# Kernel optimization log

Measured on AMD Instinct MI355X. Metric: run time of the kernel, lower is better.

The kernel has to match this reference:

```python
import jax, jax.numpy as jnp
import numpy as np

B, K, N, E, D = 32, 32, 2048, 16384, 768
L_GNN, L_TR, H = 2, 4, 12
FF, VOCAB, N_ROLES, MAX_POS, N_HOPS = 3072, 25, 2, 64, 16


def setup_inputs() -> dict:
    key = jax.random.key(0)
    ks = jax.random.split(key, 32)
    s = 0.02
    inp = {
        "raw_features": jax.random.normal(ks[0], (B, K, D), jnp.float32),
        "x0": jax.random.randint(ks[1], (K, N), 0, VOCAB),
        "edge0": jax.random.randint(ks[2], (K, 2, E), 0, N),
        "batch0": jnp.sort(jax.random.randint(ks[3], (K, N), 0, B), axis=-1),
        "x1": jax.random.randint(ks[4], (K, N), 0, VOCAB),
        "edge1": jax.random.randint(ks[5], (K, 2, E), 0, N),
        "batch1": jnp.sort(jax.random.randint(ks[6], (K, N), 0, B), axis=-1),
        "role_ids": jax.random.randint(ks[7], (B, K), 0, N_ROLES),
        "position_ids": jax.random.randint(ks[8], (B, K), 0, MAX_POS),
        "hop_ids": jax.random.randint(ks[9], (B, K), 0, N_HOPS),
        # GNNForProtein params (shared across slots and both proteins)
        "amino_embed": jax.random.normal(ks[10], (VOCAB, D)) * s,
        "gnn_W": jax.random.normal(ks[11], (L_GNN, D, D)) * s,
        "gnn_b": jnp.zeros((L_GNN, D)),
        # GraphBert embeddings
        "role_emb": jax.random.normal(ks[12], (N_ROLES, D)) * s,
        "pos_emb": jax.random.normal(ks[13], (MAX_POS, D)) * s,
        "hop_emb": jax.random.normal(ks[14], (N_HOPS, D)) * s,
        "emb_ln_scale": jnp.ones((D,)),
        "emb_ln_bias": jnp.zeros((D,)),
        # GraphBert transformer layers (stacked over L_TR)
        "Wq": jax.random.normal(ks[15], (L_TR, D, D)) * s,
        "bq": jnp.zeros((L_TR, D)),
        "Wk": jax.random.normal(ks[16], (L_TR, D, D)) * s,
        "bk": jnp.zeros((L_TR, D)),
        "Wv": jax.random.normal(ks[17], (L_TR, D, D)) * s,
        "bv": jnp.zeros((L_TR, D)),
        "Wo": jax.random.normal(ks[18], (L_TR, D, D)) * s,
        "bo": jnp.zeros((L_TR, D)),
        "ln1_s": jnp.ones((L_TR, D)),
        "ln1_b": jnp.zeros((L_TR, D)),
        "W1": jax.random.normal(ks[19], (L_TR, D, FF)) * s,
        "b1": jnp.zeros((L_TR, FF)),
        "W2": jax.random.normal(ks[20], (L_TR, FF, D)) * s,
        "b2": jnp.zeros((L_TR, D)),
        "ln2_s": jnp.ones((L_TR, D)),
        "ln2_b": jnp.zeros((L_TR, D)),
    }
    return inp


def _ln(x, s, b):
    m = jnp.mean(x, -1, keepdims=True)
    v = jnp.mean(jnp.square(x - m), -1, keepdims=True)
    return (x - m) * jax.lax.rsqrt(v + 1e-12) * s + b


def _gnn(node_ids, edges, batch_idx, amino_embed, W, b):
    # One protein slot: GCN message passing + mean readout per graph in batch.
    h = amino_embed[node_ids]                      # [N, D]
    src, dst = edges[0], edges[1]
    for l in range(W.shape[0]):
        agg = jax.ops.segment_sum(h[src], dst, num_segments=N)
        h = jax.nn.relu((h + agg) @ W[l] + b[l])
    sums = jax.ops.segment_sum(h, batch_idx, num_segments=B)
    cnt = jax.ops.segment_sum(jnp.ones((h.shape[0], 1), h.dtype), batch_idx, num_segments=B)
    return sums / jnp.maximum(cnt, 1.0)           # [B, D]


def reference(raw_features, x0, edge0, batch0, x1, edge1, batch1, role_ids, position_ids, hop_ids,
              amino_embed, gnn_W, gnn_b, role_emb, pos_emb, hop_emb, emb_ln_scale, emb_ln_bias,
              Wq, bq, Wk, bk, Wv, bv, Wo, bo, ln1_s, ln1_b, W1, b1, W2, b2, ln2_s, ln2_b):
    # vmap over the K protein slots replaces the original Python loop (same math).
    gnn_v = jax.vmap(_gnn, in_axes=(0, 0, 0, None, None, None))
    p0 = gnn_v(x0, edge0, batch0, amino_embed, gnn_W, gnn_b)   # [K, B, D]
    p1 = gnn_v(x1, edge1, batch1, amino_embed, gnn_W, gnn_b)   # [K, B, D]
    feats = raw_features + jnp.transpose(p0 + p1, (1, 0, 2))   # [B, K, D]
    # GraphBert embeddings + encoder
    h = feats + role_emb[role_ids] + pos_emb[position_ids] + hop_emb[hop_ids]
    h = _ln(h, emb_ln_scale, emb_ln_bias)
    dh = D // H
    scale = float(1.0 / np.sqrt(dh))
    for l in range(Wq.shape[0]):
        q = (h @ Wq[l] + bq[l]).reshape(B, K, H, dh)
        kk = (h @ Wk[l] + bk[l]).reshape(B, K, H, dh)
        v = (h @ Wv[l] + bv[l]).reshape(B, K, H, dh)
        att = jax.nn.softmax(jnp.einsum('bqhd,bkhd->bhqk', q, kk) * scale, axis=-1)
        ctx = jnp.einsum('bhqk,bkhd->bqhd', att, v).reshape(B, K, D)
        h = _ln(h + ctx @ Wo[l] + bo[l], ln1_s[l], ln1_b[l])
        f = jax.nn.gelu(h @ W1[l] + b1[l]) @ W2[l] + b2[l]
        h = _ln(h + f, ln2_s[l], ln2_b[l])
    return h
```

## Files before the change

kernel.cpp:

```cpp
#include <hip/hip_runtime.h>
#include <hip/hip_bf16.h>
#include <math.h>

using bf16 = __hip_bfloat16;
typedef __attribute__((ext_vector_type(8))) short short8;
typedef __attribute__((ext_vector_type(4))) float floatx4;
typedef __attribute__((ext_vector_type(4))) short short4v;

#define NB   32
#define NK   32
#define NNODE 2048
#define NEDGE 16384
#define ND   768
#define NHH  12
#define DHH  64
#define NFF  3072
#define NG   64
#define LTR  4
#define VOCAB 25

static __device__ __forceinline__ float b2f(bf16 x) { return __bfloat162float(x); }
static __device__ __forceinline__ bf16 f2b(float x) { return __float2bfloat16(x); }
static __device__ __forceinline__ float bs2f(short s) {
    unsigned u = ((unsigned)(unsigned short)s) << 16;
    float f; __builtin_memcpy(&f, &u, 4); return f;
}
static __device__ __forceinline__ short f2bs(float x) {
    bf16 h = f2b(x); short s; __builtin_memcpy(&s, &h, 2); return s;
}

static __device__ __forceinline__ void load_lds16(const bf16* g, bf16* l) {
    __builtin_amdgcn_global_load_lds((const __attribute__((address_space(1))) void*)g,
                                     (__attribute__((address_space(3))) void*)l, 16, 0, 0);
}

static __device__ __forceinline__ float ldf(const void* p, size_t i, bool f32) {
    return f32 ? ((const float*)p)[i] : b2f(((const bf16*)p)[i]);
}

__global__ void detect_dtype_kernel(const void* __restrict__ eln_s, int* __restrict__ flag) {
    if (threadIdx.x == 0 && blockIdx.x == 0) {
        unsigned w = ((const unsigned*)eln_s)[0];
        flag[0] = (w == 0x3F800000u) ? 1 : 0;
    }
}

__device__ __forceinline__ void conv_tile(const void* __restrict__ src, size_t srcOff,
                                          bf16* __restrict__ dst, int R, int Cn,
                                          int tr, int tc, bool f32, int t,
                                          bf16 (*tile)[65]) {
    int r0 = tr * 64, c0 = tc * 64;
    #pragma unroll
    for (int p = 0; p < 16; ++p) {
        int idx = t + p * 256;
        int r = idx >> 6, c = idx & 63;
        tile[r][c] = f2b(ldf(src, srcOff + (size_t)(r0 + r) * Cn + c0 + c, f32));
    }
    __syncthreads();
    #pragma unroll
    for (int p = 0; p < 16; ++p) {
        int idx = t + p * 256;
        int c = idx >> 6, r = idx & 63;
        dst[(size_t)(c0 + c) * R + r0 + r] = tile[r][c];
    }
}

__global__ __launch_bounds__(256) void convert_gnn_kernel(const void* __restrict__ gnnW,
                                                          bf16* __restrict__ gnnT,
                                                          const int* __restrict__ flag) {
    __shared__ bf16 tile[64][65];
    bool f32 = flag[0] != 0;
    int bid = blockIdx.x;
    int id = bid / 144, tl = bid % 144;
    conv_tile(gnnW, (size_t)id * 589824, gnnT + (size_t)id * 589824,
              768, 768, tl / 12, tl % 12, f32, threadIdx.x, tile);
}

__global__ __launch_bounds__(256) void convert_layer_kernel(
    const void* __restrict__ Wq, const void* __restrict__ Wk, const void* __restrict__ Wv,
    const void* __restrict__ Wo, const void* __restrict__ W1, const void* __restrict__ W2,
    int l, bf16* __restrict__ qkvT, bf16* __restrict__ oT,
    bf16* __restrict__ w1T, bf16* __restrict__ w2T, const int* __restrict__ flag) {
    __shared__ bf16 tile[64][65];
    bool f32 = flag[0] != 0;
    int bid = blockIdx.x, t = threadIdx.x;
    if (bid < 432) {
        int m = bid / 144, tl = bid % 144;
        const void* src = (m == 0) ? Wq : ((m == 1) ? Wk : Wv);
        conv_tile(src, (size_t)l * 589824, qkvT + (size_t)m * 589824,
                  768, 768, tl / 12, tl % 12, f32, t, tile);
    } else if (bid < 576) {
        int tl = bid - 432;
        conv_tile(Wo, (size_t)l * 589824, oT, 768, 768, tl / 12, tl % 12, f32, t, tile);
    } else if (bid < 1152) {
        int tl = bid - 576;
        conv_tile(W1, (size_t)l * 768 * 3072, w1T, 768, 3072, tl / 48, tl % 48, f32, t, tile);
    } else {
        int tl = bid - 1152;
        conv_tile(W2, (size_t)l * 3072 * 768, w2T, 3072, 768, tl / 12, tl % 12, f32, t, tile);
    }
}

__global__ __launch_bounds__(256) void pack_bias_kernel(
    const void* __restrict__ gnnb, const void* __restrict__ bq, const void* __restrict__ bk,
    const void* __restrict__ bv, const void* __restrict__ bo, const void* __restrict__ b1,
    const void* __restrict__ b2, float* __restrict__ out, const int* __restrict__ flag) {
    bool f32 = flag[0] != 0;
    int i = blockIdx.x * 256 + threadIdx.x;
    if (i >= 1536 + LTR * 6912) return;
    float v;
    if (i < 1536) v = ldf(gnnb, i, f32);
    else {
        int j = i - 1536, l = j / 6912, r = j % 6912;
        if      (r <  768) v = ldf(bq, l * 768 + r, f32);
        else if (r < 1536) v = ldf(bk, l * 768 + r - 768, f32);
        else if (r < 2304) v = ldf(bv, l * 768 + r - 1536, f32);
        else if (r < 3072) v = ldf(bo, l * 768 + r - 2304, f32);
        else if (r < 6144) v = ldf(b1, l * 3072 + r - 3072, f32);
        else               v = ldf(b2, l * 768 + r - 6144, f32);
    }
    out[i] = v;
}

__global__ __launch_bounds__(192) void e1_kernel(const void* __restrict__ emb,
                                                 const bf16* __restrict__ w0T,
                                                 bf16* __restrict__ E1,
                                                 const int* __restrict__ flag) {
    bool f32 = flag[0] != 0;
    int v = blockIdx.x, t = threadIdx.x;
    float acc[4] = {0.f, 0.f, 0.f, 0.f};
    for (int k = 0; k < ND; k += 4) {
        float e0 = ldf(emb, (size_t)v * ND + k,     f32);
        float e1 = ldf(emb, (size_t)v * ND + k + 1, f32);
        float e2 = ldf(emb, (size_t)v * ND + k + 2, f32);
        float e3 = ldf(emb, (size_t)v * ND + k + 3, f32);
        #pragma unroll
        for (int j = 0; j < 4; ++j) {
            const short4v w = *(const short4v*)&w0T[(size_t)(t * 4 + j) * ND + k];
            acc[j] += e0 * bs2f(w.x) + e1 * bs2f(w.y) + e2 * bs2f(w.z) + e3 * bs2f(w.w);
        }
    }
    short4v o; o.x = f2bs(acc[0]); o.y = f2bs(acc[1]); o.z = f2bs(acc[2]); o.w = f2bs(acc[3]);
    ((short4v*)(E1 + (size_t)v * ND))[t] = o;
}

__global__ __launch_bounds__(256) void count_deg_kernel(const int* __restrict__ edge0,
                                                        const int* __restrict__ edge1,
                                                        int* __restrict__ deg) {
    int gid = blockIdx.x;
    int g = gid >> 6, chunk = gid & 63;
    const int* ep = (g < NK) ? (edge0 + (size_t)g * 2 * NEDGE)
                             : (edge1 + (size_t)(g - NK) * 2 * NEDGE);
    int e = chunk * 256 + threadIdx.x;
    int dst = ep[NEDGE + e];
    atomicAdd(&deg[g * NNODE + dst], 1);
}

__global__ __launch_bounds__(256) void scan_deg_kernel(int* __restrict__ deg,
                                                       int* __restrict__ indptr) {
    int g = blockIdx.x, t = threadIdx.x;
    __shared__ int sums[256];
    int loc[8]; int s = 0;
    #pragma unroll
    for (int i = 0; i < 8; ++i) { loc[i] = deg[g * NNODE + t * 8 + i]; s += loc[i]; }
    sums[t] = s; __syncthreads();
    for (int off = 1; off < 256; off <<= 1) {
        int v = (t >= off) ? sums[t - off] : 0;
        __syncthreads();
        sums[t] += v;
        __syncthreads();
    }
    int run = sums[t] - s;
    #pragma unroll
    for (int i = 0; i < 8; ++i) {
        indptr[g * (NNODE + 1) + t * 8 + i] = run;
        deg[g * NNODE + t * 8 + i] = run;
        run += loc[i];
    }
    if (t == 255) indptr[g * (NNODE + 1) + NNODE] = run;
}

__global__ __launch_bounds__(256) void fill_csr_kernel(const int* __restrict__ edge0,
                                                       const int* __restrict__ edge1,
                                                       int* __restrict__ cursor,
                                                       int* __restrict__ csr_src) {
    int gid = blockIdx.x;
    int g = gid >> 6, chunk = gid & 63;
    const int* ep = (g < NK) ? (edge0 + (size_t)g * 2 * NEDGE)
                             : (edge1 + (size_t)(g - NK) * 2 * NEDGE);
    int e = chunk * 256 + threadIdx.x;
    int src = ep[e];
    int dst = ep[NEDGE + e];
    int p = atomicAdd(&cursor[g * NNODE + dst], 1);
    csr_src[(size_t)g * NEDGE + p] = src;
}

__global__ __launch_bounds__(64) void batch_count_kernel(const int* __restrict__ batch0,
                                                         const int* __restrict__ batch1,
                                                         int* __restrict__ cnt) {
    int g = blockIdx.x;
    int b = threadIdx.x;
    if (b >= NB) return;
    const int* bp = (g < NK) ? (batch0 + (size_t)g * NNODE)
                             : (batch1 + (size_t)(g - NK) * NNODE);
    int lo = 0, hi = NNODE;
    while (lo < hi) { int mid = (lo + hi) >> 1; if (bp[mid] < b) lo = mid + 1; else hi = mid; }
    int start = lo;
    hi = NNODE;
    while (lo < hi) { int mid = (lo + hi) >> 1; if (bp[mid] < b + 1) lo = mid + 1; else hi = mid; }
    cnt[g * NB + b] = lo - start;
}

static __device__ __forceinline__ void node_block_decode(int id, int& gl, int& n) {
    int r = id & 7, q = id >> 3;
    gl = r + 8 * (q >> 11);
    n = q & 2047;
}

__global__ __launch_bounds__(192) void gnn_layer1_kernel(const int* __restrict__ x0,
                                                         const int* __restrict__ x1,
                                                         const bf16* __restrict__ E1,
                                                         const float* __restrict__ b0,
                                                         const int* __restrict__ indptr,
                                                         const int* __restrict__ csr_src,
                                                         bf16* __restrict__ hC, int g0) {
    int gl, n; node_block_decode(blockIdx.x, gl, n);
    int g = g0 + gl;
    const int* xg = (g < NK) ? (x0 + (size_t)g * NNODE) : (x1 + (size_t)(g - NK) * NNODE);
    int beg = indptr[g * (NNODE + 1) + n];
    int end = indptr[g * (NNODE + 1) + n + 1];
    const int* cs = csr_src + (size_t)g * NEDGE;
    int t = threadIdx.x;
    const short4v* E = (const short4v*)E1;
    short4v v = E[(size_t)xg[n] * 192 + t];
    float a0 = bs2f(v.x), a1 = bs2f(v.y), a2 = bs2f(v.z), a3 = bs2f(v.w);
    for (int e = beg; e < end; ++e) {
        int s = cs[e];
        short4v w = E[(size_t)xg[s] * 192 + t];
        a0 += bs2f(w.x); a1 += bs2f(w.y); a2 += bs2f(w.z); a3 += bs2f(w.w);
    }
    float4 bb = ((const float4*)b0)[t];
    short4v o;
    o.x = f2bs(fmaxf(a0 + bb.x, 0.f));
    o.y = f2bs(fmaxf(a1 + bb.y, 0.f));
    o.z = f2bs(fmaxf(a2 + bb.z, 0.f));
    o.w = f2bs(fmaxf(a3 + bb.w, 0.f));
    ((short4v*)(hC + ((size_t)gl * NNODE + n) * ND))[t] = o;
}

__global__ __launch_bounds__(192) void gnn_aggregate_kernel(const bf16* __restrict__ hC,
                                                            const int* __restrict__ indptr,
                                                            const int* __restrict__ csr_src,
                                                            bf16* __restrict__ xC, int g0) {
    int gl, n; node_block_decode(blockIdx.x, gl, n);
    int g = g0 + gl;
    int beg = indptr[g * (NNODE + 1) + n];
    int end = indptr[g * (NNODE + 1) + n + 1];
    const short4v* hg = (const short4v*)(hC + (size_t)gl * NNODE * ND);
    const int* cs = csr_src + (size_t)g * NEDGE;
    int t = threadIdx.x;
    short4v v = hg[(size_t)n * 192 + t];
    float a0 = bs2f(v.x), a1 = bs2f(v.y), a2 = bs2f(v.z), a3 = bs2f(v.w);
    for (int e = beg; e < end; ++e) {
        int s = cs[e];
        short4v w = hg[(size_t)s * 192 + t];
        a0 += bs2f(w.x); a1 += bs2f(w.y); a2 += bs2f(w.z); a3 += bs2f(w.w);
    }
    short4v o; o.x = f2bs(a0); o.y = f2bs(a1); o.z = f2bs(a2); o.w = f2bs(a3);
    ((short4v*)(xC + ((size_t)gl * NNODE + n) * ND))[t] = o;
}

__global__ __launch_bounds__(256) void gemm_tn(const bf16* __restrict__ A,
                                               const bf16* __restrict__ BT,
                                               const float* __restrict__ bias,
                                               void* __restrict__ C,
                                               int M, int K, int N,
                                               int act, int outF32,
                                               const int* __restrict__ batAp,
                                               const int* __restrict__ batBp,
                                               float* __restrict__ pool, int g0) {
    __shared__ bf16 lA[2][128][32];
    __shared__ bf16 lB[2][128][32];
    int nTilesN = N >> 7, nTilesM = M >> 7;
    int brow, bcol;
    if ((nTilesM & 7) == 0) {
        int xcd = blockIdx.x & 7, j = blockIdx.x >> 3;
        brow = (j / nTilesN) * 8 + xcd;
        bcol = j % nTilesN;
    } else {
        bcol = blockIdx.x % nTilesN;
        brow = blockIdx.x / nTilesN;
    }
    int t = threadIdx.x;
    int wave = t >> 6, lane = t & 63;
    int wr = wave >> 1, wc = wave & 1;
    int l15 = lane & 15, quad = lane >> 4;
    const int row0 = brow << 7, col0 = bcol << 7;
    const int sr0 = t >> 2, sk0 = (t & 3) * 8;
    const bf16* Ab = A + (size_t)(row0 + sr0) * K + sk0;
    const bf16* Bb = BT + (size_t)(col0 + sr0) * K + sk0;
    const size_t rstride = (size_t)64 * K;

    load_lds16(Ab,           &lA[0][sr0][sk0]);
    load_lds16(Ab + rstride, &lA[0][sr0 + 64][sk0]);
    load_lds16(Bb,           &lB[0][sr0][sk0]);
    load_lds16(Bb + rstride, &lB[0][sr0 + 64][sk0]);

    floatx4 acc[4][4] = {};
    int cur = 0;
    for (int k0 = 0; k0 < K; k0 += 32) {
        __syncthreads();
        if (k0 + 32 < K) {
            load_lds16(Ab + k0 + 32,           &lA[cur ^ 1][sr0][sk0]);
            load_lds16(Ab + rstride + k0 + 32, &lA[cur ^ 1][sr0 + 64][sk0]);
            load_lds16(Bb + k0 + 32,           &lB[cur ^ 1][sr0][sk0]);
            load_lds16(Bb + rstride + k0 + 32, &lB[cur ^ 1][sr0 + 64][sk0]);
        }
        short8 afr[4], bfr[4];
        #pragma unroll
        for (int i = 0; i < 4; ++i)
            afr[i] = *reinterpret_cast<const short8*>(&lA[cur][wr * 64 + i * 16 + l15][quad * 8]);
        #pragma unroll
        for (int j = 0; j < 4; ++j)
            bfr[j] = *reinterpret_cast<const short8*>(&lB[cur][wc * 64 + j * 16 + l15][quad * 8]);
        #pragma unroll
        for (int i = 0; i < 4; ++i)
            #pragma unroll
            for (int j = 0; j < 4; ++j)
                acc[i][j] = __builtin_amdgcn_mfma_f32_16x16x32_bf16(afr[i], bfr[j], acc[i][j], 0, 0, 0);
        cur ^= 1;
    }

    if (pool) {
        int g = g0 + (row0 >> 11);
        const int* bp = (g < NK) ? (batAp + (size_t)g * NNODE)
                                 : (batBp + (size_t)(g - NK) * NNODE);
        int nbase = row0 & (NNODE - 1);
        float* pg = pool + (size_t)g * NB * ND;
        int cb = wc * 64 + l15;
        float bv[4];
        #pragma unroll
        for (int j = 0; j < 4; ++j) bv[j] = bias[col0 + cb + j * 16];
        __syncthreads();
        float* lp = (float*)lA;
        int bLo = bp[nbase], bHi = bp[nbase + 127];
        int nb = (bHi - bLo + 1) * 128;
        for (int idx = t; idx < nb; idx += 256) lp[idx] = 0.f;
        __syncthreads();
        float sums[4] = {0.f, 0.f, 0.f, 0.f};
        int curb = -1;
        #pragma unroll
        for (int i = 0; i < 4; ++i) {
            int rr = nbase + wr * 64 + i * 16 + quad * 4;
            #pragma unroll
            for (int r = 0; r < 4; ++r) {
                int b = bp[rr + r];
                if (b != curb) {
                    if (curb >= 0) {
                        #pragma unroll
                        for (int j = 0; j < 4; ++j)
                            atomicAdd(&lp[(curb - bLo) * 128 + cb + j * 16], sums[j]);
                    }
                    curb = b;
                    sums[0] = sums[1] = sums[2] = sums[3] = 0.f;
                }
                #pragma unroll
                for (int j = 0; j < 4; ++j) {
                    float v = acc[i][j][r] + bv[j];
                    if (act == 1) v = fmaxf(v, 0.f);
                    sums[j] += v;
                }
            }
        }
        #pragma unroll
        for (int j = 0; j < 4; ++j)
            atomicAdd(&lp[(curb - bLo) * 128 + cb + j * 16], sums[j]);
        __syncthreads();
        for (int idx = t; idx < nb; idx += 256) {
            float v = lp[idx];
            if (v != 0.f)
                atomicAdd(&pg[(size_t)(bLo + (idx >> 7)) * ND + col0 + (idx & 127)], v);
        }
        return;
    }

    #pragma unroll
    for (int i = 0; i < 4; ++i) {
        int rbase = row0 + wr * 64 + i * 16 + quad * 4;
        #pragma unroll
        for (int j = 0; j < 4; ++j) {
            int c = col0 + wc * 64 + j * 16 + l15;
            float bv = bias[c];
            #pragma unroll
            for (int r = 0; r < 4; ++r) {
                float v = acc[i][j][r] + bv;
                if (act == 1) v = fmaxf(v, 0.f);
                else if (act == 2) {
                    float x = v;
                    float u = 1.5957691216057308f * (x + 0.044715f * x * x * x);
                    v = x / (1.f + __expf(-u));
                }
                size_t idx = (size_t)(rbase + r) * N + c;
                if (outF32) ((float*)C)[idx] = v;
                else        ((bf16*)C)[idx] = f2b(v);
            }
        }
    }
}

__global__ __launch_bounds__(256) void gemm_tn_sk(const bf16* __restrict__ A,
                                                  const bf16* __restrict__ BT,
                                                  const float* __restrict__ bias,
                                                  float* __restrict__ C,
                                                  int M, int K, int N, int splitK) {
    __shared__ bf16 lA[2][64][32];
    __shared__ bf16 lB[2][128][32];
    int nTilesN = N >> 7, nTilesM = M >> 6;
    int tiles = nTilesM * nTilesN;
    int split = blockIdx.x / tiles;
    int jt = blockIdx.x % tiles;
    int brow = jt / nTilesN, bcol = jt % nTilesN;
    int t = threadIdx.x;
    int wave = t >> 6, lane = t & 63;
    int wr = wave >> 1, wc = wave & 1;
    int l15 = lane & 15, quad = lane >> 4;
    const int row0 = brow << 6, col0 = bcol << 7;
    const int kLen = K / splitK, kBeg = split * kLen;
    const int sr0 = t >> 2, sk0 = (t & 3) * 8;
    const bf16* Ab = A + (size_t)(row0 + sr0) * K + kBeg + sk0;
    const bf16* Bb = BT + (size_t)(col0 + sr0) * K + kBeg + sk0;
    const size_t rstride = (size_t)64 * K;

    load_lds16(Ab,           &lA[0][sr0][sk0]);
    load_lds16(Bb,           &lB[0][sr0][sk0]);
    load_lds16(Bb + rstride, &lB[0][sr0 + 64][sk0]);

    floatx4 acc[2][4] = {};
    int cur = 0;
    for (int k0 = 0; k0 < kLen; k0 += 32) {
        __syncthreads();
        if (k0 + 32 < kLen) {
            load_lds16(Ab + k0 + 32,           &lA[cur ^ 1][sr0][sk0]);
            load_lds16(Bb + k0 + 32,           &lB[cur ^ 1][sr0][sk0]);
            load_lds16(Bb + rstride + k0 + 32, &lB[cur ^ 1][sr0 + 64][sk0]);
        }
        short8 afr[2], bfr[4];
        #pragma unroll
        for (int i = 0; i < 2; ++i)
            afr[i] = *reinterpret_cast<const short8*>(&lA[cur][wr * 32 + i * 16 + l15][quad * 8]);
        #pragma unroll
        for (int j = 0; j < 4; ++j)
            bfr[j] = *reinterpret_cast<const short8*>(&lB[cur][wc * 64 + j * 16 + l15][quad * 8]);
        #pragma unroll
        for (int i = 0; i < 2; ++i)
            #pragma unroll
            for (int j = 0; j < 4; ++j)
                acc[i][j] = __builtin_amdgcn_mfma_f32_16x16x32_bf16(afr[i], bfr[j], acc[i][j], 0, 0, 0);
        cur ^= 1;
    }
    #pragma unroll
    for (int i = 0; i < 2; ++i) {
        int rbase = row0 + wr * 32 + i * 16 + quad * 4;
        #pragma unroll
        for (int j = 0; j < 4; ++j) {
            int c = col0 + wc * 64 + j * 16 + l15;
            float bv = (split == 0) ? bias[c] : 0.f;
            #pragma unroll
            for (int r = 0; r < 4; ++r)
                atomicAdd(&C[(size_t)(rbase + r) * N + c], acc[i][j][r] + bv);
        }
    }
}

__device__ __forceinline__ void block_ln_768(float (&x)[3], int t,
                                             const void* __restrict__ s,
                                             const void* __restrict__ b,
                                             size_t sOff, bool f32,
                                             float (&y)[3], float* red) {
    float loc = x[0] + x[1] + x[2];
    red[t] = loc; __syncthreads();
    for (int off = 128; off > 0; off >>= 1) {
        if (t < off) red[t] += red[t + off];
        __syncthreads();
    }
    float mean = red[0] * (1.f / 768.f);
    __syncthreads();
    float vs = 0.f;
    #pragma unroll
    for (int e = 0; e < 3; ++e) { float d = x[e] - mean; vs += d * d; }
    red[t] = vs; __syncthreads();
    for (int off = 128; off > 0; off >>= 1) {
        if (t < off) red[t] += red[t + off];
        __syncthreads();
    }
    float var = red[0] * (1.f / 768.f);
    __syncthreads();
    float inv = rsqrtf(var + 1e-12f);
    #pragma unroll
    for (int e = 0; e < 3; ++e) {
        int d = t + e * 256;
        y[e] = (x[e] - mean) * inv * ldf(s, sOff + d, f32) + ldf(b, sOff + d, f32);
    }
}

__global__ __launch_bounds__(256) void combine_embed_ln_kernel(
    const void* __restrict__ raw, const float* __restrict__ pooled,
    const int* __restrict__ cnt,
    const int* __restrict__ role_ids, const int* __restrict__ pos_ids, const int* __restrict__ hop_ids,
    const void* __restrict__ role_emb, const void* __restrict__ pos_emb, const void* __restrict__ hop_emb,
    const void* __restrict__ lns, const void* __restrict__ lnb,
    float* __restrict__ hT, bf16* __restrict__ hbf,
    const int* __restrict__ flag) {
    bool f32 = flag[0] != 0;
    __shared__ float red[256];
    int token = blockIdx.x;
    int b = token >> 5, k = token & 31;
    int t = threadIdx.x;
    int rid = role_ids[b * NK + k];
    int pid = pos_ids[b * NK + k];
    int hid = hop_ids[b * NK + k];
    float inv0 = 1.f / (float)max(cnt[k * NB + b], 1);
    float inv1 = 1.f / (float)max(cnt[(NK + k) * NB + b], 1);
    float x[3], y[3];
    #pragma unroll
    for (int e = 0; e < 3; ++e) {
        int d = t + e * 256;
        float p0 = pooled[((size_t)k * NB + b) * ND + d] * inv0;
        float p1 = pooled[((size_t)(NK + k) * NB + b) * ND + d] * inv1;
        x[e] = ldf(raw, (size_t)token * ND + d, f32) + p0 + p1
             + ldf(role_emb, (size_t)rid * ND + d, f32)
             + ldf(pos_emb, (size_t)pid * ND + d, f32)
             + ldf(hop_emb, (size_t)hid * ND + d, f32);
    }
    block_ln_768(x, t, lns, lnb, 0, f32, y, red);
    #pragma unroll
    for (int e = 0; e < 3; ++e) {
        int d = t + e * 256;
        hT[(size_t)token * ND + d] = y[e];
        hbf[(size_t)token * ND + d] = f2b(y[e]);
    }
}

__global__ __launch_bounds__(256) void add_ln_kernel(float* __restrict__ hT,
                                                     const float* __restrict__ addv,
                                                     const void* __restrict__ lns,
                                                     const void* __restrict__ lnb,
                                                     unsigned long long sOff,
                                                     void* __restrict__ outp, int extOut,
                                                     const int* __restrict__ flag) {
    bool f32 = flag[0] != 0;
    __shared__ float red[256];
    int token = blockIdx.x;
    int t = threadIdx.x;
    float x[3], y[3];
    #pragma unroll
    for (int e = 0; e < 3; ++e) {
        int d = t + e * 256;
        x[e] = hT[(size_t)token * ND + d] + addv[(size_t)token * ND + d];
    }
    block_ln_768(x, t, lns, lnb, sOff, f32, y, red);
    #pragma unroll
    for (int e = 0; e < 3; ++e) {
        int d = t + e * 256;
        size_t idx = (size_t)token * ND + d;
        hT[idx] = y[e];
        if (extOut && f32) ((float*)outp)[idx] = y[e];
        else               ((bf16*)outp)[idx] = f2b(y[e]);
    }
}

__global__ __launch_bounds__(256) void attn_kernel(const bf16* __restrict__ qkv,
                                                   bf16* __restrict__ ctx) {
    int blk = blockIdx.x;
    int b = blk / NHH, h = blk % NHH;
    __shared__ float lq[NK][DHH], lk[NK][DHH], lv[NK][DHH];
    __shared__ float ls[NK][NK];
    int t = threadIdx.x;
    for (int i = t; i < NK * DHH; i += 256) {
        int tok = i >> 6, d = i & 63;
        size_t base = ((size_t)(b * NK + tok)) * (3 * ND) + h * DHH + d;
        lq[tok][d] = b2f(qkv[base]);
        lk[tok][d] = b2f(qkv[base + ND]);
        lv[tok][d] = b2f(qkv[base + 2 * ND]);
    }
    __syncthreads();
    const float scale = 0.125f;
    for (int i = t; i < NK * NK; i += 256) {
        int qi = i >> 5, kj = i & 31;
        float s = 0.f;
        #pragma unroll
        for (int d = 0; d < DHH; ++d) s += lq[qi][d] * lk[kj][d];
        ls[qi][kj] = s * scale;
    }
    __syncthreads();
    if (t < NK) {
        float m = -1e30f;
        for (int j = 0; j < NK; ++j) m = fmaxf(m, ls[t][j]);
        float sum = 0.f;
        for (int j = 0; j < NK; ++j) { float e = expf(ls[t][j] - m); ls[t][j] = e; sum += e; }
        float inv = 1.f / sum;
        for (int j = 0; j < NK; ++j) ls[t][j] *= inv;
    }
    __syncthreads();
    for (int i = t; i < NK * DHH; i += 256) {
        int qi = i >> 6, d = i & 63;
        float s = 0.f;
        #pragma unroll
        for (int j = 0; j < NK; ++j) s += ls[qi][j] * lv[j][d];
        ctx[((size_t)(b * NK + qi)) * ND + h * DHH + d] = f2b(s);
    }
}

extern "C" void kernel_launch(void* const* d_in, const int* in_sizes, int n_in,
                              void* d_out, int out_size, void* d_ws, size_t ws_size,
                              hipStream_t stream) {
    const void* raw      = d_in[0];
    const int*  x0       = (const int*)d_in[1];
    const int*  edge0    = (const int*)d_in[2];
    const int*  batch0   = (const int*)d_in[3];
    const int*  x1       = (const int*)d_in[4];
    const int*  edge1    = (const int*)d_in[5];
    const int*  batch1   = (const int*)d_in[6];
    const int*  role_ids = (const int*)d_in[7];
    const int*  pos_ids  = (const int*)d_in[8];
    const int*  hop_ids  = (const int*)d_in[9];
    const void* amino    = d_in[10];
    const void* gnnW     = d_in[11];
    const void* gnnb     = d_in[12];
    const void* role_emb = d_in[13];
    const void* pos_emb  = d_in[14];
    const void* hop_emb  = d_in[15];
    const void* eln_s    = d_in[16];
    const void* eln_b    = d_in[17];
    const void* Wq       = d_in[18];
    const void* bq       = d_in[19];
    const void* Wk       = d_in[20];
    const void* bk       = d_in[21];
    const void* Wv       = d_in[22];
    const void* bv       = d_in[23];
    const void* Wo       = d_in[24];
    const void* bo       = d_in[25];
    const void* ln1_s    = d_in[26];
    const void* ln1_b    = d_in[27];
    const void* W1       = d_in[28];
    const void* b1       = d_in[29];
    const void* W2       = d_in[30];
    const void* b2       = d_in[31];
    const void* ln2_s    = d_in[32];
    const void* ln2_b    = d_in[33];

    char* ws = (char*)d_ws;
    size_t off = 0;
    auto alloc = [&](size_t bytes) -> void* {
        void* p = ws + off;
        off = (off + bytes + 255) & ~(size_t)255;
        return p;
    };
    int*   dflag   = (int*)alloc(256);
    float* pooled  = (float*)alloc((size_t)NG * NB * ND * 4);
    int*   cntb    = (int*)alloc((size_t)NG * NB * 4);
    int*   indptr  = (int*)alloc((size_t)NG * (NNODE + 1) * 4);
    int*   csr_src = (int*)alloc((size_t)NG * NEDGE * 4);
    int*   degcur  = (int*)alloc((size_t)NG * NNODE * 4);
    bf16*  gnnT    = (bf16*)alloc((size_t)2 * ND * ND * 2);
    bf16*  E1      = (bf16*)alloc((size_t)VOCAB * ND * 2);
    float* biasPk  = (float*)alloc((size_t)(1536 + LTR * 6912) * 4);

    const size_t QS = (size_t)3 * ND * ND, OS = (size_t)ND * ND;
    const size_t S1 = (size_t)ND * NFF,    S2 = (size_t)NFF * ND;
    const size_t wPerLayer = (QS + OS + S1 + S2) * 2;
    const size_t perG  = (size_t)NNODE * ND * 2;
    const size_t bigTR = 21 * 1024 * 1024;
    int gc = 8, nlw = 1;
    for (int cand = 32; cand >= 8; cand >>= 1) {
        size_t bigGNN = 2 * (size_t)cand * perG;
        size_t big = bigGNN > bigTR ? bigGNN : bigTR;
        if (off + 4 * wPerLayer + big + (1 << 20) <= ws_size) { gc = cand; nlw = 4; break; }
        if (off + wPerLayer + big + (1 << 20) <= ws_size)     { gc = cand; nlw = 1; break; }
    }
    bf16* qkvT = (bf16*)alloc(QS * 2 * nlw);
    bf16* oT   = (bf16*)alloc(OS * 2 * nlw);
    bf16* w1T  = (bf16*)alloc(S1 * 2 * nlw);
    bf16* w2T  = (bf16*)alloc(S2 * 2 * nlw);

    char* bigbase = (char*)alloc(2 * (size_t)gc * perG > bigTR ? 2 * (size_t)gc * perG : bigTR);
    bf16* hC = (bf16*)bigbase;
    bf16* xC = (bf16*)(bigbase + (size_t)gc * perG);
    size_t toff = 0;
    auto talloc = [&](size_t bytes) -> void* {
        void* p = bigbase + toff;
        toff = (toff + bytes + 255) & ~(size_t)255;
        return p;
    };
    float* hT    = (float*)talloc((size_t)NB * NK * ND * 4);
    bf16*  hbf   = (bf16*)talloc((size_t)NB * NK * ND * 2);
    bf16*  qkvb  = (bf16*)talloc((size_t)NB * NK * 3 * ND * 2);
    bf16*  ctxb  = (bf16*)talloc((size_t)NB * NK * ND * 2);
    float* resid = (float*)talloc((size_t)NB * NK * ND * 4);
    bf16*  ffbuf = (bf16*)talloc((size_t)NB * NK * NFF * 2);

    auto gemm = [&](const bf16* A, const bf16* BT, const float* bias, void* C,
                    int Mm, int Kk, int Nn, int act, int outF32) {
        int blocks = (Mm >> 7) * (Nn >> 7);
        gemm_tn<<<blocks, 256, 0, stream>>>(A, BT, bias, C, Mm, Kk, Nn, act, outF32,
                                            nullptr, nullptr, nullptr, 0);
    };
    auto gemm_sk = [&](const bf16* A, const bf16* BT, const float* bias, float* C,
                       int Mm, int Kk, int Nn, int splitK) {
        hipMemsetAsync(C, 0, (size_t)Mm * Nn * 4, stream);
        int blocks = (Mm >> 6) * (Nn >> 7) * splitK;
        gemm_tn_sk<<<blocks, 256, 0, stream>>>(A, BT, bias, C, Mm, Kk, Nn, splitK);
    };

    detect_dtype_kernel<<<1, 64, 0, stream>>>(eln_s, dflag);

    convert_gnn_kernel<<<288, 256, 0, stream>>>(gnnW, gnnT, dflag);
    pack_bias_kernel<<<(1536 + LTR * 6912 + 255) / 256, 256, 0, stream>>>(
        gnnb, bq, bk, bv, bo, b1, b2, biasPk, dflag);
    e1_kernel<<<VOCAB, 192, 0, stream>>>(amino, gnnT, E1, dflag);
    if (nlw == 4)
        for (int l = 0; l < LTR; ++l)
            convert_layer_kernel<<<1728, 256, 0, stream>>>(
                Wq, Wk, Wv, Wo, W1, W2, l,
                qkvT + (size_t)l * QS, oT + (size_t)l * OS,
                w1T + (size_t)l * S1, w2T + (size_t)l * S2, dflag);

    hipMemsetAsync(degcur, 0, (size_t)NG * NNODE * 4, stream);
    hipMemsetAsync(pooled, 0, (size_t)NG * NB * ND * 4, stream);
    count_deg_kernel<<<NG * 64, 256, 0, stream>>>(edge0, edge1, degcur);
    scan_deg_kernel<<<NG, 256, 0, stream>>>(degcur, indptr);
    fill_csr_kernel<<<NG * 64, 256, 0, stream>>>(edge0, edge1, degcur, csr_src);
    batch_count_kernel<<<NG, 64, 0, stream>>>(batch0, batch1, cntb);

    for (int g0 = 0; g0 < NG; g0 += gc) {
        gnn_layer1_kernel<<<gc * NNODE, 192, 0, stream>>>(x0, x1, E1, biasPk,
                                                          indptr, csr_src, hC, g0);
        gnn_aggregate_kernel<<<gc * NNODE, 192, 0, stream>>>(hC, indptr, csr_src, xC, g0);
        int blocks = ((gc * NNODE) >> 7) * (ND >> 7);
        gemm_tn<<<blocks, 256, 0, stream>>>(xC, gnnT + (size_t)ND * ND, biasPk + ND, nullptr,
                                            gc * NNODE, ND, ND, 1, 0,
                                            batch0, batch1, pooled, g0);
    }

    combine_embed_ln_kernel<<<NB * NK, 256, 0, stream>>>(
        raw, pooled, cntb, role_ids, pos_ids, hop_ids,
        role_emb, pos_emb, hop_emb, eln_s, eln_b, hT, hbf, dflag);

    const int M = NB * NK;
    for (int l = 0; l < LTR; ++l) {
        bf16* qkvTl = qkvT + (size_t)(nlw == 4 ? l : 0) * QS;
        bf16* oTl   = oT   + (size_t)(nlw == 4 ? l : 0) * OS;
        bf16* w1Tl  = w1T  + (size_t)(nlw == 4 ? l : 0) * S1;
        bf16* w2Tl  = w2T  + (size_t)(nlw == 4 ? l : 0) * S2;
        if (nlw == 1)
            convert_layer_kernel<<<1728, 256, 0, stream>>>(Wq, Wk, Wv, Wo, W1, W2, l,
                                                           qkvTl, oTl, w1Tl, w2Tl, dflag);
        const float* lb = biasPk + 1536 + l * 6912;
        gemm(hbf, qkvTl, lb, qkvb, M, ND, 3 * ND, 0, 0);
        attn_kernel<<<NB * NHH, 256, 0, stream>>>(qkvb, ctxb);
        gemm_sk(ctxb, oTl, lb + 2304, resid, M, ND, ND, 2);
        add_ln_kernel<<<M, 256, 0, stream>>>(hT, resid, ln1_s, ln1_b,
                                             (unsigned long long)l * ND, hbf, 0, dflag);
        gemm(hbf, w1Tl, lb + 3072, ffbuf, M, ND, NFF, 2, 0);
        gemm_sk(ffbuf, w2Tl, lb + 6144, resid, M, NFF, ND, 4);
        int ext = (l == LTR - 1) ? 1 : 0;
        void* outb = ext ? d_out : (void*)hbf;
        add_ln_kernel<<<M, 256, 0, stream>>>(hT, resid, ln2_s, ln2_b,
                                             (unsigned long long)l * ND, outb, ext, dflag);
    }
}
```

Measured before the change: 1.439 ms.

## Vectorize weight transpose, accumulate residual in-place, use 64-row GEMM for transformer

The weight-transpose tile kernel now does vectorized 4-wide loads and stores through a padded short tile instead of scalar accesses. Split-K GEMMs now atomically add straight into the residual hidden-state buffer, so the separate residual buffer, its memset and the extra add in layer norm go away. The QKV and FF1 GEMMs switch to the 64-row tile kernel with fused activation and bf16 store, which gives more blocks for M=1024. The attention load uses 8-wide vector reads, and per-layer weight conversion always runs inside the layer loop rather than being hoisted when workspace allowed, so conversion can no longer overlap earlier work.

```diff
diff --git a/kernel.cpp b/kernel.cpp
--- a/kernel.cpp
+++ b/kernel.cpp
@@ -48,27 +48,38 @@
 __device__ __forceinline__ void conv_tile(const void* __restrict__ src, size_t srcOff,
                                           bf16* __restrict__ dst, int R, int Cn,
                                           int tr, int tc, bool f32, int t,
-                                          bf16 (*tile)[65]) {
+                                          short (*tile)[70]) {
     int r0 = tr * 64, c0 = tc * 64;
-    #pragma unroll
-    for (int p = 0; p < 16; ++p) {
-        int idx = t + p * 256;
-        int r = idx >> 6, c = idx & 63;
-        tile[r][c] = f2b(ldf(src, srcOff + (size_t)(r0 + r) * Cn + c0 + c, f32));
+    int rr = t >> 4, c4 = (t & 15) * 4;
+    #pragma unroll
+    for (int p = 0; p < 4; ++p) {
+        int r = rr + p * 16;
+        size_t base = srcOff + (size_t)(r0 + r) * Cn + c0 + c4;
+        short4v s;
+        if (f32) {
+            float4 v = *(const float4*)((const float*)src + base);
+            s.x = f2bs(v.x); s.y = f2bs(v.y); s.z = f2bs(v.z); s.w = f2bs(v.w);
+        } else {
+            s = *(const short4v*)((const short*)src + base);
+        }
+        tile[r][c4]     = s.x; tile[r][c4 + 1] = s.y;
+        tile[r][c4 + 2] = s.z; tile[r][c4 + 3] = s.w;
     }
     __syncthreads();
     #pragma unroll
-    for (int p = 0; p < 16; ++p) {
-        int idx = t + p * 256;
-        int c = idx >> 6, r = idx & 63;
-        dst[(size_t)(c0 + c) * R + r0 + r] = tile[r][c];
+    for (int p = 0; p < 4; ++p) {
+        int c = rr + p * 16;
+        short4v o;
+        o.x = tile[c4][c];     o.y = tile[c4 + 1][c];
+        o.z = tile[c4 + 2][c]; o.w = tile[c4 + 3][c];
+        *(short4v*)((short*)dst + (size_t)(c0 + c) * R + r0 + c4) = o;
     }
 }
 
 __global__ __launch_bounds__(256) void convert_gnn_kernel(const void* __restrict__ gnnW,
                                                           bf16* __restrict__ gnnT,
                                                           const int* __restrict__ flag) {
-    __shared__ bf16 tile[64][65];
+    __shared__ short tile[64][70];
     bool f32 = flag[0] != 0;
     int bid = blockIdx.x;
     int id = bid / 144, tl = bid % 144;
@@ -81,7 +92,7 @@
     const void* __restrict__ Wo, const void* __restrict__ W1, const void* __restrict__ W2,
     int l, bf16* __restrict__ qkvT, bf16* __restrict__ oT,
     bf16* __restrict__ w1T, bf16* __restrict__ w2T, const int* __restrict__ flag) {
-    __shared__ bf16 tile[64][65];
+    __shared__ short tile[64][70];
     bool f32 = flag[0] != 0;
     int bid = blockIdx.x, t = threadIdx.x;
     if (bid < 432) {
@@ -411,8 +422,9 @@
 __global__ __launch_bounds__(256) void gemm_tn_sk(const bf16* __restrict__ A,
                                                   const bf16* __restrict__ BT,
                                                   const float* __restrict__ bias,
-                                                  float* __restrict__ C,
-                                                  int M, int K, int N, int splitK) {
+                                                  void* __restrict__ C,
+                                                  int M, int K, int N, int splitK,
+                                                  int act, int store) {
     __shared__ bf16 lA[2][64][32];
     __shared__ bf16 lB[2][128][32];
     int nTilesN = N >> 7, nTilesM = M >> 6;
@@ -466,8 +478,19 @@
             int c = col0 + wc * 64 + j * 16 + l15;
             float bv = (split == 0) ? bias[c] : 0.f;
             #pragma unroll
-            for (int r = 0; r < 4; ++r)
-                atomicAdd(&C[(size_t)(rbase + r) * N + c], acc[i][j][r] + bv);
+            for (int r = 0; r < 4; ++r) {
+                float v = acc[i][j][r] + bv;
+                if (act == 1) v = fmaxf(v, 0.f);
+                else if (act == 2) {
+                    float x = v;
+                    float u = 1.5957691216057308f * (x + 0.044715f * x * x * x);
+                    v = x / (1.f + __expf(-u));
+                }
+                size_t idx = (size_t)(rbase + r) * N + c;
+                if (store == 0)      atomicAdd(&((float*)C)[idx], v);
+                else if (store == 1) ((float*)C)[idx] = v;
+                else                 ((bf16*)C)[idx] = f2b(v);
+            }
         }
     }
 }
@@ -542,7 +565,6 @@
 }
 
 __global__ __launch_bounds__(256) void add_ln_kernel(float* __restrict__ hT,
-                                                     const float* __restrict__ addv,
                                                      const void* __restrict__ lns,
                                                      const void* __restrict__ lnb,
                                                      unsigned long long sOff,
@@ -556,7 +578,7 @@
     #pragma unroll
     for (int e = 0; e < 3; ++e) {
         int d = t + e * 256;
-        x[e] = hT[(size_t)token * ND + d] + addv[(size_t)token * ND + d];
+        x[e] = hT[(size_t)token * ND + d];
     }
     block_ln_768(x, t, lns, lnb, sOff, f32, y, red);
     #pragma unroll
@@ -576,12 +598,18 @@
     __shared__ float lq[NK][DHH], lk[NK][DHH], lv[NK][DHH];
     __shared__ float ls[NK][NK];
     int t = threadIdx.x;
-    for (int i = t; i < NK * DHH; i += 256) {
-        int tok = i >> 6, d = i & 63;
-        size_t base = ((size_t)(b * NK + tok)) * (3 * ND) + h * DHH + d;
-        lq[tok][d] = b2f(qkv[base]);
-        lk[tok][d] = b2f(qkv[base + ND]);
-        lv[tok][d] = b2f(qkv[base + 2 * ND]);
+    {
+        int tok = t >> 3, d8 = (t & 7) * 8;
+        size_t base = ((size_t)(b * NK + tok)) * (3 * ND) + h * DHH + d8;
+        short8 q8 = *(const short8*)&qkv[base];
+        short8 k8 = *(const short8*)&qkv[base + ND];
+        short8 v8 = *(const short8*)&qkv[base + 2 * ND];
+        #pragma unroll
+        for (int j = 0; j < 8; ++j) {
+            lq[tok][d8 + j] = bs2f(q8[j]);
+            lk[tok][d8 + j] = bs2f(k8[j]);
+            lv[tok][d8 + j] = bs2f(v8[j]);
+        }
     }
     __syncthreads();
     const float scale = 0.125f;
@@ -665,24 +693,21 @@
     bf16*  gnnT    = (bf16*)alloc((size_t)2 * ND * ND * 2);
     bf16*  E1      = (bf16*)alloc((size_t)VOCAB * ND * 2);
     float* biasPk  = (float*)alloc((size_t)(1536 + LTR * 6912) * 4);
-
     const size_t QS = (size_t)3 * ND * ND, OS = (size_t)ND * ND;
     const size_t S1 = (size_t)ND * NFF,    S2 = (size_t)NFF * ND;
-    const size_t wPerLayer = (QS + OS + S1 + S2) * 2;
+    bf16*  qkvT    = (bf16*)alloc(QS * 2);
+    bf16*  oT      = (bf16*)alloc(OS * 2);
+    bf16*  w1T     = (bf16*)alloc(S1 * 2);
+    bf16*  w2T     = (bf16*)alloc(S2 * 2);
+
     const size_t perG  = (size_t)NNODE * ND * 2;
     const size_t bigTR = 21 * 1024 * 1024;
-    int gc = 8, nlw = 1;
+    int gc = 8;
     for (int cand = 32; cand >= 8; cand >>= 1) {
         size_t bigGNN = 2 * (size_t)cand * perG;
-        size_t big = bigGNN > bigTR ? bigGNN : bigTR;
-        if (off + 4 * wPerLayer + big + (1 << 20) <= ws_size) { gc = cand; nlw = 4; break; }
-        if (off + wPerLayer + big + (1 << 20) <= ws_size)     { gc = cand; nlw = 1; break; }
-    }
-    bf16* qkvT = (bf16*)alloc(QS * 2 * nlw);
-    bf16* oT   = (bf16*)alloc(OS * 2 * nlw);
-    bf16* w1T  = (bf16*)alloc(S1 * 2 * nlw);
-    bf16* w2T  = (bf16*)alloc(S2 * 2 * nlw);
-
+        size_t need = off + (bigGNN > bigTR ? bigGNN : bigTR) + (1 << 20);
+        if (need <= ws_size) { gc = cand; break; }
+    }
     char* bigbase = (char*)alloc(2 * (size_t)gc * perG > bigTR ? 2 * (size_t)gc * perG : bigTR);
     bf16* hC = (bf16*)bigbase;
     bf16* xC = (bf16*)(bigbase + (size_t)gc * perG);
@@ -696,20 +721,12 @@
     bf16*  hbf   = (bf16*)talloc((size_t)NB * NK * ND * 2);
     bf16*  qkvb  = (bf16*)talloc((size_t)NB * NK * 3 * ND * 2);
     bf16*  ctxb  = (bf16*)talloc((size_t)NB * NK * ND * 2);
-    float* resid = (float*)talloc((size_t)NB * NK * ND * 4);
     bf16*  ffbuf = (bf16*)talloc((size_t)NB * NK * NFF * 2);
 
-    auto gemm = [&](const bf16* A, const bf16* BT, const float* bias, void* C,
-                    int Mm, int Kk, int Nn, int act, int outF32) {
-        int blocks = (Mm >> 7) * (Nn >> 7);
-        gemm_tn<<<blocks, 256, 0, stream>>>(A, BT, bias, C, Mm, Kk, Nn, act, outF32,
-                                            nullptr, nullptr, nullptr, 0);
-    };
-    auto gemm_sk = [&](const bf16* A, const bf16* BT, const float* bias, float* C,
-                       int Mm, int Kk, int Nn, int splitK) {
-        hipMemsetAsync(C, 0, (size_t)Mm * Nn * 4, stream);
+    auto gemm_sk = [&](const bf16* A, const bf16* BT, const float* bias, void* C,
+                       int Mm, int Kk, int Nn, int splitK, int act, int store) {
         int blocks = (Mm >> 6) * (Nn >> 7) * splitK;
-        gemm_tn_sk<<<blocks, 256, 0, stream>>>(A, BT, bias, C, Mm, Kk, Nn, splitK);
+        gemm_tn_sk<<<blocks, 256, 0, stream>>>(A, BT, bias, C, Mm, Kk, Nn, splitK, act, store);
     };
 
     detect_dtype_kernel<<<1, 64, 0, stream>>>(eln_s, dflag);
@@ -718,12 +735,6 @@
     pack_bias_kernel<<<(1536 + LTR * 6912 + 255) / 256, 256, 0, stream>>>(
         gnnb, bq, bk, bv, bo, b1, b2, biasPk, dflag);
     e1_kernel<<<VOCAB, 192, 0, stream>>>(amino, gnnT, E1, dflag);
-    if (nlw == 4)
-        for (int l = 0; l < LTR; ++l)
-            convert_layer_kernel<<<1728, 256, 0, stream>>>(
-                Wq, Wk, Wv, Wo, W1, W2, l,
-                qkvT + (size_t)l * QS, oT + (size_t)l * OS,
-                w1T + (size_t)l * S1, w2T + (size_t)l * S2, dflag);
 
     hipMemsetAsync(degcur, 0, (size_t)NG * NNODE * 4, stream);
     hipMemsetAsync(pooled, 0, (size_t)NG * NB * ND * 4, stream);
@@ -748,24 +759,19 @@
 
     const int M = NB * NK;
     for (int l = 0; l < LTR; ++l) {
-        bf16* qkvTl = qkvT + (size_t)(nlw == 4 ? l : 0) * QS;
-        bf16* oTl   = oT   + (size_t)(nlw == 4 ? l : 0) * OS;
-        bf16* w1Tl  = w1T  + (size_t)(nlw == 4 ? l : 0) * S1;
-        bf16* w2Tl  = w2T  + (size_t)(nlw == 4 ? l : 0) * S2;
-        if (nlw == 1)
-            convert_layer_kernel<<<1728, 256, 0, stream>>>(Wq, Wk, Wv, Wo, W1, W2, l,
-                                                           qkvTl, oTl, w1Tl, w2Tl, dflag);
+        convert_layer_kernel<<<1728, 256, 0, stream>>>(Wq, Wk, Wv, Wo, W1, W2, l,
+                                                       qkvT, oT, w1T, w2T, dflag);
         const float* lb = biasPk + 1536 + l * 6912;
-        gemm(hbf, qkvTl, lb, qkvb, M, ND, 3 * ND, 0, 0);
+        gemm_sk(hbf, qkvT, lb, qkvb, M, ND, 3 * ND, 1, 0, 2);
         attn_kernel<<<NB * NHH, 256, 0, stream>>>(qkvb, ctxb);
-        gemm_sk(ctxb, oTl, lb + 2304, resid, M, ND, ND, 2);
-        add_ln_kernel<<<M, 256, 0, stream>>>(hT, resid, ln1_s, ln1_b,
+        gemm_sk(ctxb, oT, lb + 2304, hT, M, ND, ND, 2, 0, 0);
+        add_ln_kernel<<<M, 256, 0, stream>>>(hT, ln1_s, ln1_b,
                                              (unsigned long long)l * ND, hbf, 0, dflag);
-        gemm(hbf, w1Tl, lb + 3072, ffbuf, M, ND, NFF, 2, 0);
-        gemm_sk(ffbuf, w2Tl, lb + 6144, resid, M, NFF, ND, 4);
+        gemm_sk(hbf, w1T, lb + 3072, ffbuf, M, ND, NFF, 1, 2, 2);
+        gemm_sk(ffbuf, w2T, lb + 6144, hT, M, NFF, ND, 4, 0, 0);
         int ext = (l == LTR - 1) ? 1 : 0;
         void* outb = ext ? d_out : (void*)hbf;
-        add_ln_kernel<<<M, 256, 0, stream>>>(hT, resid, ln2_s, ln2_b,
+        add_ln_kernel<<<M, 256, 0, stream>>>(hT, ln2_s, ln2_b,
                                              (unsigned long long)l * ND, outb, ext, dflag);
     }
 }
```

Measured after the change: 1.374 ms. 1.05x faster.
